# Optimization experiments

Measured on AMD Instinct MI355X. Metric: run time of the kernel, lower is better.

Reference implementation:

```python
import jax, jax.numpy as jnp
import numpy as np

B, S, D = 2, 2048, 768
H = 12
HD = D // H


def setup_inputs() -> dict:
    key = jax.random.key(0)
    ks = jax.random.split(key, 9)
    s_in = 1.0 / np.sqrt(D)
    return {
        "x": jax.random.normal(ks[0], (B, S, D), dtype=jnp.float32),
        "wq": jax.random.normal(ks[1], (D, D), dtype=jnp.float32) * s_in,
        "bq": jax.random.normal(ks[2], (D,), dtype=jnp.float32) * 0.01,
        "wk": jax.random.normal(ks[3], (D, D), dtype=jnp.float32) * s_in,
        "bk": jax.random.normal(ks[4], (D,), dtype=jnp.float32) * 0.01,
        "wv": jax.random.normal(ks[5], (D, D), dtype=jnp.float32) * s_in,
        "bv": jax.random.normal(ks[6], (D,), dtype=jnp.float32) * 0.01,
        "wo": jax.random.normal(ks[7], (D, D), dtype=jnp.float32) * s_in,
        "bo": jax.random.normal(ks[8], (D,), dtype=jnp.float32) * 0.01,
    }


def reference(x, wq, bq, wk, bk, wv, bv, wo, bo):
    b, s, _ = x.shape
    # projections -> [b, h, s, hd]
    def proj(w, bias):
        return (x @ w + bias).reshape(b, s, H, HD).transpose(0, 2, 1, 3)
    q = proj(wq, bq)
    k = proj(wk, bk)
    v = proj(wv, bv)
    scores = jnp.einsum("bhqd,bhkd->bhqk", q, k)
    causal = jnp.triu(jnp.ones((s, s), dtype=bool), k=1)
    scores = jnp.where(causal, -jnp.inf, scores)
    attn = jax.nn.softmax(scores / np.sqrt(HD), axis=-1)
    # dropout p=0.0 -> identity
    ctx = jnp.einsum("bhqk,bhkd->bhqd", attn, v)
    ctx = ctx.transpose(0, 2, 1, 3).reshape(b, s, D)
    return ctx @ wo + bo
```

## Files before the change

### kernel.cpp

```cpp
#include <hip/hip_runtime.h>
#include <math.h>

#define BB  2
#define SS  2048
#define DD  768
#define HH  12
#define HDD 64
#define BSR (BB * SS)
#define NCH 40
#define NKT 12

typedef __attribute__((ext_vector_type(8))) short bf16x8;
typedef __attribute__((ext_vector_type(4))) float f32x4;
typedef __attribute__((ext_vector_type(4))) int  i32x4;

__device__ inline f32x4 mfma16(bf16x8 a, bf16x8 b, f32x4 c) {
    return __builtin_amdgcn_mfma_f32_16x16x32_bf16(a, b, c, 0, 0, 0);
}

__device__ inline unsigned short f2b(float f) {
    unsigned int u = __float_as_uint(f);
    u += 0x7FFFu + ((u >> 16) & 1u);
    return (unsigned short)(u >> 16);
}
__device__ inline float b2f(unsigned short u) {
    return __uint_as_float((unsigned int)u << 16);
}

__device__ inline unsigned int cvt_pk_bf16(float lo, float hi) {
    unsigned int r;
    asm("v_cvt_pk_bf16_f32 %0, %1, %2" : "=v"(r) : "v"(lo), "v"(hi));
    return r;
}

__device__ inline void async_copy16(void* lds, const void* g) {
    __builtin_amdgcn_global_load_lds(
        (const __attribute__((address_space(1))) unsigned int*)g,
        (__attribute__((address_space(3))) unsigned int*)lds, 16, 0, 0);
}

__global__ __launch_bounds__(256) void conv_wT_kernel(
    const float* __restrict__ w0, const float* __restrict__ w1,
    const float* __restrict__ w2, const float* __restrict__ w3,
    unsigned short* __restrict__ o0, unsigned short* __restrict__ o1,
    unsigned short* __restrict__ o2, unsigned short* __restrict__ o3)
{
    const float* w = (blockIdx.z == 0) ? w0 : (blockIdx.z == 1) ? w1
                   : (blockIdx.z == 2) ? w2 : w3;
    unsigned short* o = (blockIdx.z == 0) ? o0 : (blockIdx.z == 1) ? o1
                      : (blockIdx.z == 2) ? o2 : o3;
    const int n0 = blockIdx.x * 64;
    const int k0 = blockIdx.y * 64;
    const int tid = threadIdx.x;

    __shared__ unsigned short tile[64][72];

#pragma unroll
    for (int p = 0; p < 4; ++p) {
        int c  = p * 256 + tid;
        int kr = c >> 4;
        int nc = (c & 15) * 4;
        float4 v = *(const float4*)&w[(size_t)(k0 + kr) * DD + n0 + nc];
        tile[nc + 0][kr] = f2b(v.x);
        tile[nc + 1][kr] = f2b(v.y);
        tile[nc + 2][kr] = f2b(v.z);
        tile[nc + 3][kr] = f2b(v.w);
    }
    __syncthreads();
#pragma unroll
    for (int p = 0; p < 2; ++p) {
        int c  = p * 256 + tid;
        int nr = c >> 3;
        int kc = (c & 7) * 8;
        *(i32x4*)&o[(size_t)(n0 + nr) * DD + k0 + kc] = *(const i32x4*)&tile[nr][kc];
    }
}

__global__ __launch_bounds__(256) void qkv_gemm_kernel(
    const float* __restrict__ x,
    const unsigned short* __restrict__ wqT, const unsigned short* __restrict__ wkT,
    const unsigned short* __restrict__ wvT,
    const float* __restrict__ bq, const float* __restrict__ bk,
    const float* __restrict__ bv,
    unsigned short* __restrict__ Qg, unsigned short* __restrict__ Kg,
    unsigned short* __restrict__ Vg)
{
    const int which = blockIdx.z;
    const unsigned short* Bt = (which == 0) ? wqT : (which == 1) ? wkT : wvT;
    const float* bias        = (which == 0) ? bq  : (which == 1) ? bk  : bv;
    unsigned short* out      = (which == 0) ? Qg  : (which == 1) ? Kg  : Vg;
    const float qs           = (which == 0) ? 0.18033688011112042f : 1.0f;

    const int m0 = blockIdx.x * 64;
    const int n0 = blockIdx.y * 128;
    const int tid  = threadIdx.x;
    const int w    = tid >> 6;
    const int lane = tid & 63;
    const int quad = lane >> 4;
    const int l16  = lane & 15;
    const int mh   = w & 1;
    const int nh   = w >> 1;
    const int swz  = l16 & 7;

    __shared__ unsigned short smem[24576];
    unsigned short (*As0)[64] = (unsigned short(*)[64])smem;
    unsigned short (*Bs0)[64] = (unsigned short(*)[64])(smem + 4096);
    unsigned short (*As1)[64] = (unsigned short(*)[64])(smem + 12288);
    unsigned short (*Bs1)[64] = (unsigned short(*)[64])(smem + 16384);
    unsigned short (*T)[136]  = (unsigned short(*)[136])smem;

    const int rA0 = tid >> 3,          jA0 = tid & 7,          chA0 = jA0 ^ (rA0 & 7);
    const int rA1 = (256 + tid) >> 3,  jA1 = tid & 7,          chA1 = jA1 ^ (rA1 & 7);
    const float* xr0 = &x[(size_t)(m0 + rA0) * DD + chA0 * 8];
    const float* xr1 = &x[(size_t)(m0 + rA1) * DD + chA1 * 8];
    int ldsA0 = rA0 * 64 + jA0 * 8;
    int ldsA1 = rA1 * 64 + jA1 * 8;

    const unsigned short* gB[4];
    int ldsB[4];
#pragma unroll
    for (int p = 0; p < 4; ++p) {
        int c  = p * 256 + tid;
        int r  = c >> 3;
        int j  = c & 7;
        int ch = j ^ (r & 7);
        gB[p]   = &Bt[(size_t)(n0 + r) * DD + ch * 8];
        ldsB[p] = r * 64 + j * 8;
    }

    f32x4 zero = {0.f, 0.f, 0.f, 0.f};
    f32x4 acc[2][4];
#pragma unroll
    for (int i = 0; i < 2; ++i)
#pragma unroll
        for (int j = 0; j < 4; ++j) acc[i][j] = zero;

    {
        float4 pf0 = *(const float4*)(xr0);
        float4 pf1 = *(const float4*)(xr0 + 4);
        float4 pf2 = *(const float4*)(xr1);
        float4 pf3 = *(const float4*)(xr1 + 4);
#pragma unroll
        for (int p = 0; p < 4; ++p)
            async_copy16((unsigned short*)Bs0 + ldsB[p], gB[p]);
        i32x4 tv;
        tv[0] = (int)cvt_pk_bf16(pf0.x, pf0.y);
        tv[1] = (int)cvt_pk_bf16(pf0.z, pf0.w);
        tv[2] = (int)cvt_pk_bf16(pf1.x, pf1.y);
        tv[3] = (int)cvt_pk_bf16(pf1.z, pf1.w);
        *(i32x4*)((unsigned short*)As0 + ldsA0) = tv;
        tv[0] = (int)cvt_pk_bf16(pf2.x, pf2.y);
        tv[1] = (int)cvt_pk_bf16(pf2.z, pf2.w);
        tv[2] = (int)cvt_pk_bf16(pf3.x, pf3.y);
        tv[3] = (int)cvt_pk_bf16(pf3.z, pf3.w);
        *(i32x4*)((unsigned short*)As0 + ldsA1) = tv;
    }
    __syncthreads();

#pragma unroll
    for (int t = 0; t < NKT; ++t) {
        const int kn = (t + 1) * 64;
        unsigned short (*As)[64] = (t & 1) ? As1 : As0;
        unsigned short (*Bs)[64] = (t & 1) ? Bs1 : Bs0;
        unsigned short (*An)[64] = (t & 1) ? As0 : As1;
        unsigned short (*Bn)[64] = (t & 1) ? Bs0 : Bs1;
        const bool more = (t + 1 < NKT);

        float4 pf0, pf1, pf2, pf3;
        if (more) {
            pf0 = *(const float4*)(xr0 + kn);
            pf1 = *(const float4*)(xr0 + kn + 4);
            pf2 = *(const float4*)(xr1 + kn);
            pf3 = *(const float4*)(xr1 + kn + 4);
#pragma unroll
            for (int p = 0; p < 4; ++p)
                async_copy16((unsigned short*)Bn + ldsB[p], gB[p] + kn);
        }

        bf16x8 af0[2], af1[2], bf0[4], bf1[4];
#pragma unroll
        for (int mt = 0; mt < 2; ++mt) {
            int r = mh * 32 + mt * 16 + l16;
            af0[mt] = *(const bf16x8*)&As[r][((quad    ) ^ swz) * 8];
            af1[mt] = *(const bf16x8*)&As[r][((quad + 4) ^ swz) * 8];
        }
#pragma unroll
        for (int nt = 0; nt < 4; ++nt) {
            int r = nh * 64 + nt * 16 + l16;
            bf0[nt] = *(const bf16x8*)&Bs[r][((quad    ) ^ swz) * 8];
            bf1[nt] = *(const bf16x8*)&Bs[r][((quad + 4) ^ swz) * 8];
        }
#pragma unroll
        for (int mt = 0; mt < 2; ++mt)
#pragma unroll
            for (int nt = 0; nt < 4; ++nt) {
                acc[mt][nt] = mfma16(af0[mt], bf0[nt], acc[mt][nt]);
                acc[mt][nt] = mfma16(af1[mt], bf1[nt], acc[mt][nt]);
            }

        if (more) {
            i32x4 tv;
            tv[0] = (int)cvt_pk_bf16(pf0.x, pf0.y);
            tv[1] = (int)cvt_pk_bf16(pf0.z, pf0.w);
            tv[2] = (int)cvt_pk_bf16(pf1.x, pf1.y);
            tv[3] = (int)cvt_pk_bf16(pf1.z, pf1.w);
            *(i32x4*)((unsigned short*)An + ldsA0) = tv;
            tv[0] = (int)cvt_pk_bf16(pf2.x, pf2.y);
            tv[1] = (int)cvt_pk_bf16(pf2.z, pf2.w);
            tv[2] = (int)cvt_pk_bf16(pf3.x, pf3.y);
            tv[3] = (int)cvt_pk_bf16(pf3.z, pf3.w);
            *(i32x4*)((unsigned short*)An + ldsA1) = tv;
        }
        __syncthreads();
    }

    if (which < 2) {
#pragma unroll
        for (int nt = 0; nt < 4; ++nt) {
            const int col = nh * 64 + nt * 16 + l16;
            const float bvv = bias[n0 + col];
#pragma unroll
            for (int mt = 0; mt < 2; ++mt)
#pragma unroll
                for (int r = 0; r < 4; ++r)
                    T[mh * 32 + mt * 16 + quad * 4 + r][col] =
                        f2b((acc[mt][nt][r] + bvv) * qs);
        }
        __syncthreads();
#pragma unroll
        for (int p2 = 0; p2 < 4; ++p2) {
            int c    = p2 * 256 + tid;
            int row  = c >> 4;
            int ck   = c & 15;
            int head = ck >> 3;
            int wi   = ck & 7;
            int sg   = m0 + row;
            int bi   = sg >> 11, si = sg & 2047;
            int hcol = (n0 >> 6) + head;
            *(i32x4*)&out[(((size_t)(bi * HH + hcol)) * SS + si) * HDD + wi * 8] =
                *(const i32x4*)&T[row][head * 64 + wi * 8];
        }
    } else {
        for (int pass = 0; pass < 2; ++pass) {
            if (pass) __syncthreads();
            if (nh == pass) {
#pragma unroll
                for (int nt = 0; nt < 4; ++nt) {
                    const float bvv = bias[n0 + pass * 64 + nt * 16 + l16];
#pragma unroll
                    for (int mt = 0; mt < 2; ++mt) {
                        uint2 pk;
                        pk.x = cvt_pk_bf16(acc[mt][nt][0] + bvv, acc[mt][nt][1] + bvv);
                        pk.y = cvt_pk_bf16(acc[mt][nt][2] + bvv, acc[mt][nt][3] + bvv);
                        *(uint2*)&T[nt * 16 + l16][mh * 32 + mt * 16 + quad * 4] = pk;
                    }
                }
            }
            __syncthreads();
            const int bi   = m0 >> 11;
            const int s0   = m0 & 2047;
            const int hcol = (n0 >> 6) + pass;
#pragma unroll
            for (int p2 = 0; p2 < 2; ++p2) {
                int c    = p2 * 256 + tid;
                int drow = c >> 3;
                int wi   = c & 7;
                *(i32x4*)&out[(((size_t)(bi * HH + hcol)) * HDD + drow) * SS + s0 + wi * 8] =
                    *(const i32x4*)&T[drow][wi * 8];
            }
        }
    }
}

__global__ __launch_bounds__(256) void out_gemm_kernel(
    const unsigned short* __restrict__ cb, const unsigned short* __restrict__ woT,
    const float* __restrict__ bo, float* __restrict__ out)
{
    const int m0 = blockIdx.x * 64;
    const int n0 = blockIdx.y * 128;
    const int tid  = threadIdx.x;
    const int w    = tid >> 6;
    const int lane = tid & 63;
    const int quad = lane >> 4;
    const int l16  = lane & 15;
    const int mh   = w & 1;
    const int nh   = w >> 1;
    const int swz  = l16 & 7;

    __shared__ unsigned short smem[24576];
    unsigned short (*As0)[64] = (unsigned short(*)[64])smem;
    unsigned short (*Bs0)[64] = (unsigned short(*)[64])(smem + 4096);
    unsigned short (*As1)[64] = (unsigned short(*)[64])(smem + 12288);
    unsigned short (*Bs1)[64] = (unsigned short(*)[64])(smem + 16384);

    const unsigned short* gA[2];
    int ldsA[2];
#pragma unroll
    for (int p = 0; p < 2; ++p) {
        int c  = p * 256 + tid;
        int r  = c >> 3;
        int j  = c & 7;
        int ch = j ^ (r & 7);
        gA[p]   = &cb[(size_t)(m0 + r) * DD + ch * 8];
        ldsA[p] = r * 64 + j * 8;
    }
    const unsigned short* gB[4];
    int ldsB[4];
#pragma unroll
    for (int p = 0; p < 4; ++p) {
        int c  = p * 256 + tid;
        int r  = c >> 3;
        int j  = c & 7;
        int ch = j ^ (r & 7);
        gB[p]   = &woT[(size_t)(n0 + r) * DD + ch * 8];
        ldsB[p] = r * 64 + j * 8;
    }

    f32x4 zero = {0.f, 0.f, 0.f, 0.f};
    f32x4 acc[2][4];
#pragma unroll
    for (int i = 0; i < 2; ++i)
#pragma unroll
        for (int j = 0; j < 4; ++j) acc[i][j] = zero;

#pragma unroll
    for (int p = 0; p < 2; ++p) async_copy16((unsigned short*)As0 + ldsA[p], gA[p]);
#pragma unroll
    for (int p = 0; p < 4; ++p) async_copy16((unsigned short*)Bs0 + ldsB[p], gB[p]);
    __syncthreads();

#pragma unroll
    for (int t = 0; t < NKT; ++t) {
        const int kn = (t + 1) * 64;
        unsigned short (*As)[64] = (t & 1) ? As1 : As0;
        unsigned short (*Bs)[64] = (t & 1) ? Bs1 : Bs0;
        unsigned short (*An)[64] = (t & 1) ? As0 : As1;
        unsigned short (*Bn)[64] = (t & 1) ? Bs0 : Bs1;
        if (t + 1 < NKT) {
#pragma unroll
            for (int p = 0; p < 2; ++p)
                async_copy16((unsigned short*)An + ldsA[p], gA[p] + kn);
#pragma unroll
            for (int p = 0; p < 4; ++p)
                async_copy16((unsigned short*)Bn + ldsB[p], gB[p] + kn);
        }
        bf16x8 af0[2], af1[2], bf0[4], bf1[4];
#pragma unroll
        for (int mt = 0; mt < 2; ++mt) {
            int r = mh * 32 + mt * 16 + l16;
            af0[mt] = *(const bf16x8*)&As[r][((quad    ) ^ swz) * 8];
            af1[mt] = *(const bf16x8*)&As[r][((quad + 4) ^ swz) * 8];
        }
#pragma unroll
        for (int nt = 0; nt < 4; ++nt) {
            int r = nh * 64 + nt * 16 + l16;
            bf0[nt] = *(const bf16x8*)&Bs[r][((quad    ) ^ swz) * 8];
            bf1[nt] = *(const bf16x8*)&Bs[r][((quad + 4) ^ swz) * 8];
        }
#pragma unroll
        for (int mt = 0; mt < 2; ++mt)
#pragma unroll
            for (int nt = 0; nt < 4; ++nt) {
                acc[mt][nt] = mfma16(af0[mt], bf0[nt], acc[mt][nt]);
                acc[mt][nt] = mfma16(af1[mt], bf1[nt], acc[mt][nt]);
            }
        __syncthreads();
    }

#pragma unroll
    for (int nt = 0; nt < 4; ++nt) {
        const int n = n0 + nh * 64 + nt * 16 + l16;
        const float bvv = bo[n];
#pragma unroll
        for (int mt = 0; mt < 2; ++mt) {
            const int mbase = m0 + mh * 32 + mt * 16 + quad * 4;
#pragma unroll
            for (int r = 0; r < 4; ++r)
                out[(size_t)(mbase + r) * DD + n] = acc[mt][nt][r] + bvv;
        }
    }
}

__global__ __launch_bounds__(256, 4) void attn_mfma_kernel(
    const unsigned short* __restrict__ Qg, const unsigned short* __restrict__ Kg,
    const unsigned short* __restrict__ Vg, unsigned short* __restrict__ Opart,
    float* __restrict__ Lb)
{
    const int c = (NCH - 1) - blockIdx.x;
    int qt, ck, nch;
    if (c < 4)       { qt = c;                            ck = 0;     nch = 1; }
    else if (c < 12) { int t = c - 4;  qt = 4  + (t >> 1); ck = t & 1; nch = 2; }
    else if (c < 24) { int t = c - 12; qt = 8  + t / 3;    ck = t % 3; nch = 3; }
    else             { int t = c - 24; qt = 12 + (t >> 2); ck = t & 3; nch = 4; }
    const int NT   = 2 * qt + 2;
    const int base = NT / nch, rem = NT % nch;
    const int lo   = ck * base + min(ck, rem);
    const int hi   = lo + base + (ck < rem ? 1 : 0);
    const int dlo  = 2 * qt;

    const int h  = blockIdx.y;
    const int b  = blockIdx.z;
    const int tid  = threadIdx.x;
    const int w    = tid >> 6;
    const int lane = tid & 63;
    const int quad = lane >> 4;
    const int l16  = lane & 15;
    const int q0   = qt * 128;

    const size_t bh = (size_t)(b * HH + h);
    const unsigned short* qp = Qg + bh * SS * HDD;
    const unsigned short* kp = Kg + bh * SS * HDD;
    const unsigned short* vp = Vg + bh * HDD * SS;

    unsigned short* op = Opart + ((size_t)bh * NCH + c) * 128 * HDD;
    float* lp = Lb + ((size_t)bh * NCH + c) * 128;

    __shared__ unsigned short Ks[64][64];
    __shared__ unsigned short Vt[64][64];
    __shared__ unsigned short PsT[4][2][16][72];
    unsigned short* slab = &PsT[w][0][0][0];

    bf16x8 qb0[2], qb1[2];
    int query[2];
#pragma unroll
    for (int qf = 0; qf < 2; ++qf) {
        query[qf] = q0 + w * 32 + qf * 16 + l16;
        qb0[qf] = *(const bf16x8*)&qp[(size_t)query[qf] * HDD + quad * 8];
        qb1[qf] = *(const bf16x8*)&qp[(size_t)query[qf] * HDD + 32 + quad * 8];
    }

    const int pr  = tid >> 3;
    const int po8 = tid & 7;
    const int fs  = l16 & 7;

    i32x4 kpre[2], vpre[2];
#pragma unroll
    for (int p = 0; p < 2; ++p) {
        int r  = pr + p * 32;
        int gc = (po8 ^ (r & 7)) * 8;
        kpre[p] = *(const i32x4*)&kp[(size_t)(lo * 64 + r) * HDD + gc];
        vpre[p] = *(const i32x4*)&vp[(size_t)r * SS + lo * 64 + gc];
    }

    f32x4 zero = {0.f, 0.f, 0.f, 0.f};
    f32x4 o_acc[2][4];
    float l_i[2] = {0.f, 0.f};
#pragma unroll
    for (int qf = 0; qf < 2; ++qf)
#pragma unroll
        for (int i = 0; i < 4; ++i) o_acc[qf][i] = zero;

    for (int kt = lo; kt < hi; ++kt) {
        const int k0 = kt * 64;
        __syncthreads();
#pragma unroll
        for (int p = 0; p < 2; ++p) {
            int r = pr + p * 32;
            *(i32x4*)&Ks[r][po8 * 8] = kpre[p];
            *(i32x4*)&Vt[r][po8 * 8] = vpre[p];
        }
        __syncthreads();

        if (kt + 1 < hi) {
            const int kn = (kt + 1) * 64;
#pragma unroll
            for (int p = 0; p < 2; ++p) {
                int r  = pr + p * 32;
                int gc = (po8 ^ (r & 7)) * 8;
                kpre[p] = *(const i32x4*)&kp[(size_t)(kn + r) * HDD + gc];
                vpre[p] = *(const i32x4*)&vp[(size_t)r * SS + kn + gc];
            }
        }

        const bool diag = (kt >= dlo);
#pragma unroll
        for (int t = 0; t < 4; ++t) {
            const int row = t * 16 + l16;
            bf16x8 klo = *(const bf16x8*)&Ks[row][((quad    ) ^ fs) * 8];
            bf16x8 khi = *(const bf16x8*)&Ks[row][((quad + 4) ^ fs) * 8];
#pragma unroll
            for (int qf = 0; qf < 2; ++qf) {
                f32x4 s = mfma16(klo, qb0[qf], zero);
                s = mfma16(khi, qb1[qf], s);
                float pv[4];
#pragma unroll
                for (int r = 0; r < 4; ++r) {
                    const int key = k0 + t * 16 + quad * 4 + r;
                    float p = exp2f(s[r]);
                    if (diag && key > query[qf]) p = 0.f;
                    pv[r] = p;
                    l_i[qf] += p;
                }
                uint2 pk;
                pk.x = cvt_pk_bf16(pv[0], pv[1]);
                pk.y = cvt_pk_bf16(pv[2], pv[3]);
                *(uint2*)&slab[(qf * 16 + l16) * 72 + t * 16 + quad * 4] = pk;
            }
        }

        bf16x8 pb0[2], pb1[2];
#pragma unroll
        for (int qf = 0; qf < 2; ++qf) {
            pb0[qf] = *(const bf16x8*)&slab[(qf * 16 + l16) * 72 + quad * 8];
            pb1[qf] = *(const bf16x8*)&slab[(qf * 16 + l16) * 72 + 32 + quad * 8];
        }
#pragma unroll
        for (int t2 = 0; t2 < 4; ++t2) {
            const int row = t2 * 16 + l16;
            bf16x8 vlo = *(const bf16x8*)&Vt[row][((quad    ) ^ fs) * 8];
            bf16x8 vhi = *(const bf16x8*)&Vt[row][((quad + 4) ^ fs) * 8];
#pragma unroll
            for (int qf = 0; qf < 2; ++qf) {
                o_acc[qf][t2] = mfma16(vlo, pb0[qf], o_acc[qf][t2]);
                o_acc[qf][t2] = mfma16(vhi, pb1[qf], o_acc[qf][t2]);
            }
        }
    }

#pragma unroll
    for (int qf = 0; qf < 2; ++qf) {
        float l = l_i[qf];
        l += __shfl_xor(l, 16);
        l += __shfl_xor(l, 32);
        if (quad == 0) lp[w * 32 + qf * 16 + l16] = l;
#pragma unroll
        for (int t2 = 0; t2 < 4; ++t2) {
            uint2 pk;
            pk.x = cvt_pk_bf16(o_acc[qf][t2][0], o_acc[qf][t2][1]);
            pk.y = cvt_pk_bf16(o_acc[qf][t2][2], o_acc[qf][t2][3]);
            *(uint2*)&slab[(qf * 16 + l16) * 72 + t2 * 16 + quad * 4] = pk;
        }
    }
#pragma unroll
    for (int p2 = 0; p2 < 4; ++p2) {
        int cc  = p2 * 64 + lane;
        int row = cc >> 3, dc = cc & 7;
        *(i32x4*)&op[(size_t)(w * 32 + row) * HDD + dc * 8] =
            *(const i32x4*)&slab[row * 72 + dc * 8];
    }
}

__global__ __launch_bounds__(256) void merge_kernel(
    const unsigned short* __restrict__ Opart, const float* __restrict__ Lb,
    unsigned short* __restrict__ cb)
{
    const int bx   = blockIdx.x;
    const int qt2  = bx >> 1;
    const int half = bx & 1;
    const int bhn  = blockIdx.y;
    const int b    = bhn / HH, h = bhn % HH;
    const int tid  = threadIdx.x;
    const int row  = tid >> 2;
    const int d0   = (tid & 3) * 16;
    const int rowc = half * 64 + row;
    const int q    = qt2 * 128 + rowc;

    const int nch = (qt2 < 4) ? 1 : (qt2 < 8) ? 2 : (qt2 < 12) ? 3 : 4;
    const int cb0 = (qt2 < 4) ? qt2
                  : (qt2 < 8)  ? (4  + (qt2 - 4)  * 2)
                  : (qt2 < 12) ? (12 + (qt2 - 8)  * 3)
                  :              (24 + (qt2 - 12) * 4);

    float suml = 0.f;
    float accv[16];
#pragma unroll
    for (int i = 0; i < 16; ++i) accv[i] = 0.f;

    for (int ci = 0; ci < nch; ++ci) {
        const size_t base = (size_t)bhn * NCH + cb0 + ci;
        suml += Lb[base * 128 + rowc];
        const unsigned short* o = Opart + (base * 128 + rowc) * HDD + d0;
        i32x4 va = *(const i32x4*)&o[0];
        i32x4 vb = *(const i32x4*)&o[8];
#pragma unroll
        for (int wd = 0; wd < 4; ++wd) {
            unsigned int ua = (unsigned int)va[wd];
            accv[wd * 2 + 0] += __uint_as_float(ua << 16);
            accv[wd * 2 + 1] += __uint_as_float(ua & 0xffff0000u);
            unsigned int ub = (unsigned int)vb[wd];
            accv[8 + wd * 2 + 0] += __uint_as_float(ub << 16);
            accv[8 + wd * 2 + 1] += __uint_as_float(ub & 0xffff0000u);
        }
    }
    const float inv = 1.0f / suml;
    unsigned int res[8];
#pragma unroll
    for (int i = 0; i < 8; ++i)
        res[i] = cvt_pk_bf16(accv[2 * i] * inv, accv[2 * i + 1] * inv);
    unsigned short* dst = &cb[((size_t)(b * SS + q)) * DD + h * HDD + d0];
    *(i32x4*)&dst[0] = *(const i32x4*)&res[0];
    *(i32x4*)&dst[8] = *(const i32x4*)&res[4];
}

extern "C" void kernel_launch(void* const* d_in, const int* in_sizes, int n_in,
                              void* d_out, int out_size, void* d_ws, size_t ws_size,
                              hipStream_t stream)
{
    const float* x  = (const float*)d_in[0];
    const float* wq = (const float*)d_in[1];
    const float* bq = (const float*)d_in[2];
    const float* wk = (const float*)d_in[3];
    const float* bk = (const float*)d_in[4];
    const float* wv = (const float*)d_in[5];
    const float* bv = (const float*)d_in[6];
    const float* wo = (const float*)d_in[7];
    const float* bo = (const float*)d_in[8];
    float* out = (float*)d_out;

    char* p = (char*)d_ws;
    const size_t XB  = (size_t)BSR * DD * 2;
    const size_t WB  = (size_t)DD * DD * 2;
    const size_t OPB = (size_t)BB * HH * NCH * 128 * HDD * 2;
    const size_t LBB = (size_t)BB * HH * NCH * 128 * 4;
    unsigned short* wqT = (unsigned short*)p;            p += WB;
    unsigned short* wkT = (unsigned short*)p;            p += WB;
    unsigned short* wvT = (unsigned short*)p;            p += WB;
    unsigned short* woT = (unsigned short*)p;            p += WB;
    unsigned short* Qg  = (unsigned short*)p;            p += XB;
    unsigned short* Kg  = (unsigned short*)p;            p += XB;
    unsigned short* Vg  = (unsigned short*)p;            p += XB;
    unsigned short* cb  = (unsigned short*)p;            p += XB;
    unsigned short* Opart = (unsigned short*)p;          p += OPB;
    float* Lb = (float*)p;                               p += LBB;

    conv_wT_kernel<<<dim3(DD / 64, DD / 64, 4), 256, 0, stream>>>(
        wq, wk, wv, wo, wqT, wkT, wvT, woT);
    qkv_gemm_kernel<<<dim3(BSR / 64, DD / 128, 3), 256, 0, stream>>>(
        x, wqT, wkT, wvT, bq, bk, bv, Qg, Kg, Vg);
    attn_mfma_kernel<<<dim3(NCH, HH, BB), 256, 0, stream>>>(
        Qg, Kg, Vg, Opart, Lb);
    merge_kernel<<<dim3(32, BB * HH), 256, 0, stream>>>(Opart, Lb, cb);
    out_gemm_kernel<<<dim3(BSR / 64, DD / 128), 256, 0, stream>>>(cb, woT, bo, out);
}
```

Before: 162.9 us.

## Pre-convert x to bf16 and remap GEMM/attention blocks for XCD locality

Adds a separate kernel that converts x to bf16 once, so the QKV GEMM can load A tiles with async global-to-LDS copies instead of converting float registers inside the loop. It also flattens the grids of the QKV GEMM, attention and output GEMM kernels. Block IDs are remapped so that consecutive blocks on the same XCD share M tiles or batch-head slices, aiming for better L2 reuse. The cost is one extra launch and an extra round trip of x through memory.

```diff
diff --git a/kernel.cpp b/kernel.cpp
--- a/kernel.cpp
+++ b/kernel.cpp
@@ -37,6 +37,20 @@
     __builtin_amdgcn_global_load_lds(
         (const __attribute__((address_space(1))) unsigned int*)g,
         (__attribute__((address_space(3))) unsigned int*)lds, 16, 0, 0);
+}
+
+__global__ __launch_bounds__(256) void conv_x_kernel(
+    const float* __restrict__ x, unsigned short* __restrict__ xb)
+{
+    const size_t i = ((size_t)blockIdx.x * 256 + threadIdx.x) * 8;
+    float4 f0 = *(const float4*)&x[i];
+    float4 f1 = *(const float4*)&x[i + 4];
+    i32x4 tv;
+    tv[0] = (int)cvt_pk_bf16(f0.x, f0.y);
+    tv[1] = (int)cvt_pk_bf16(f0.z, f0.w);
+    tv[2] = (int)cvt_pk_bf16(f1.x, f1.y);
+    tv[3] = (int)cvt_pk_bf16(f1.z, f1.w);
+    *(i32x4*)&xb[i] = tv;
 }
 
 __global__ __launch_bounds__(256) void conv_wT_kernel(
@@ -77,7 +91,7 @@
 }
 
 __global__ __launch_bounds__(256) void qkv_gemm_kernel(
-    const float* __restrict__ x,
+    const unsigned short* __restrict__ xb,
     const unsigned short* __restrict__ wqT, const unsigned short* __restrict__ wkT,
     const unsigned short* __restrict__ wvT,
     const float* __restrict__ bq, const float* __restrict__ bk,
@@ -85,14 +99,21 @@
     unsigned short* __restrict__ Qg, unsigned short* __restrict__ Kg,
     unsigned short* __restrict__ Vg)
 {
-    const int which = blockIdx.z;
+    const int p0   = blockIdx.x;
+    const int xcd  = p0 & 7;
+    const int slot = p0 >> 3;
+    const int m_t  = (slot / 18) * 8 + xcd;
+    const int nw   = slot % 18;
+    const int n_t  = nw / 3;
+    const int which = nw % 3;
+
     const unsigned short* Bt = (which == 0) ? wqT : (which == 1) ? wkT : wvT;
     const float* bias        = (which == 0) ? bq  : (which == 1) ? bk  : bv;
     unsigned short* out      = (which == 0) ? Qg  : (which == 1) ? Kg  : Vg;
     const float qs           = (which == 0) ? 0.18033688011112042f : 1.0f;
 
-    const int m0 = blockIdx.x * 64;
-    const int n0 = blockIdx.y * 128;
+    const int m0 = m_t * 64;
+    const int n0 = n_t * 128;
     const int tid  = threadIdx.x;
     const int w    = tid >> 6;
     const int lane = tid & 63;
@@ -109,13 +130,17 @@
     unsigned short (*Bs1)[64] = (unsigned short(*)[64])(smem + 16384);
     unsigned short (*T)[136]  = (unsigned short(*)[136])smem;
 
-    const int rA0 = tid >> 3,          jA0 = tid & 7,          chA0 = jA0 ^ (rA0 & 7);
-    const int rA1 = (256 + tid) >> 3,  jA1 = tid & 7,          chA1 = jA1 ^ (rA1 & 7);
-    const float* xr0 = &x[(size_t)(m0 + rA0) * DD + chA0 * 8];
-    const float* xr1 = &x[(size_t)(m0 + rA1) * DD + chA1 * 8];
-    int ldsA0 = rA0 * 64 + jA0 * 8;
-    int ldsA1 = rA1 * 64 + jA1 * 8;
-
+    const unsigned short* gA[2];
+    int ldsA[2];
+#pragma unroll
+    for (int p = 0; p < 2; ++p) {
+        int c  = p * 256 + tid;
+        int r  = c >> 3;
+        int j  = c & 7;
+        int ch = j ^ (r & 7);
+        gA[p]   = &xb[(size_t)(m0 + r) * DD + ch * 8];
+        ldsA[p] = r * 64 + j * 8;
+    }
     const unsigned short* gB[4];
     int ldsB[4];
 #pragma unroll
@@ -135,26 +160,10 @@
 #pragma unroll
         for (int j = 0; j < 4; ++j) acc[i][j] = zero;
 
-    {
-        float4 pf0 = *(const float4*)(xr0);
-        float4 pf1 = *(const float4*)(xr0 + 4);
-        float4 pf2 = *(const float4*)(xr1);
-        float4 pf3 = *(const float4*)(xr1 + 4);
-#pragma unroll
-        for (int p = 0; p < 4; ++p)
-            async_copy16((unsigned short*)Bs0 + ldsB[p], gB[p]);
-        i32x4 tv;
-        tv[0] = (int)cvt_pk_bf16(pf0.x, pf0.y);
-        tv[1] = (int)cvt_pk_bf16(pf0.z, pf0.w);
-        tv[2] = (int)cvt_pk_bf16(pf1.x, pf1.y);
-        tv[3] = (int)cvt_pk_bf16(pf1.z, pf1.w);
-        *(i32x4*)((unsigned short*)As0 + ldsA0) = tv;
-        tv[0] = (int)cvt_pk_bf16(pf2.x, pf2.y);
-        tv[1] = (int)cvt_pk_bf16(pf2.z, pf2.w);
-        tv[2] = (int)cvt_pk_bf16(pf3.x, pf3.y);
-        tv[3] = (int)cvt_pk_bf16(pf3.z, pf3.w);
-        *(i32x4*)((unsigned short*)As0 + ldsA1) = tv;
-    }
+#pragma unroll
+    for (int p = 0; p < 2; ++p) async_copy16((unsigned short*)As0 + ldsA[p], gA[p]);
+#pragma unroll
+    for (int p = 0; p < 4; ++p) async_copy16((unsigned short*)Bs0 + ldsB[p], gB[p]);
     __syncthreads();
 
 #pragma unroll
@@ -164,19 +173,14 @@
         unsigned short (*Bs)[64] = (t & 1) ? Bs1 : Bs0;
         unsigned short (*An)[64] = (t & 1) ? As0 : As1;
         unsigned short (*Bn)[64] = (t & 1) ? Bs0 : Bs1;
-        const bool more = (t + 1 < NKT);
-
-        float4 pf0, pf1, pf2, pf3;
-        if (more) {
-            pf0 = *(const float4*)(xr0 + kn);
-            pf1 = *(const float4*)(xr0 + kn + 4);
-            pf2 = *(const float4*)(xr1 + kn);
-            pf3 = *(const float4*)(xr1 + kn + 4);
+        if (t + 1 < NKT) {
+#pragma unroll
+            for (int p = 0; p < 2; ++p)
+                async_copy16((unsigned short*)An + ldsA[p], gA[p] + kn);
 #pragma unroll
             for (int p = 0; p < 4; ++p)
                 async_copy16((unsigned short*)Bn + ldsB[p], gB[p] + kn);
         }
-
         bf16x8 af0[2], af1[2], bf0[4], bf1[4];
 #pragma unroll
         for (int mt = 0; mt < 2; ++mt) {
@@ -197,20 +201,6 @@
                 acc[mt][nt] = mfma16(af0[mt], bf0[nt], acc[mt][nt]);
                 acc[mt][nt] = mfma16(af1[mt], bf1[nt], acc[mt][nt]);
             }
-
-        if (more) {
-            i32x4 tv;
-            tv[0] = (int)cvt_pk_bf16(pf0.x, pf0.y);
-            tv[1] = (int)cvt_pk_bf16(pf0.z, pf0.w);
-            tv[2] = (int)cvt_pk_bf16(pf1.x, pf1.y);
-            tv[3] = (int)cvt_pk_bf16(pf1.z, pf1.w);
-            *(i32x4*)((unsigned short*)An + ldsA0) = tv;
-            tv[0] = (int)cvt_pk_bf16(pf2.x, pf2.y);
-            tv[1] = (int)cvt_pk_bf16(pf2.z, pf2.w);
-            tv[2] = (int)cvt_pk_bf16(pf3.x, pf3.y);
-            tv[3] = (int)cvt_pk_bf16(pf3.z, pf3.w);
-            *(i32x4*)((unsigned short*)An + ldsA1) = tv;
-        }
         __syncthreads();
     }
 
@@ -276,8 +266,11 @@
     const unsigned short* __restrict__ cb, const unsigned short* __restrict__ woT,
     const float* __restrict__ bo, float* __restrict__ out)
 {
-    const int m0 = blockIdx.x * 64;
-    const int n0 = blockIdx.y * 128;
+    const int p0   = blockIdx.x;
+    const int xcd  = p0 & 7;
+    const int slot = p0 >> 3;
+    const int m0 = ((slot / 6) * 8 + xcd) * 64;
+    const int n0 = (slot % 6) * 128;
     const int tid  = threadIdx.x;
     const int w    = tid >> 6;
     const int lane = tid & 63;
@@ -386,7 +379,14 @@
     const unsigned short* __restrict__ Vg, unsigned short* __restrict__ Opart,
     float* __restrict__ Lb)
 {
-    const int c = (NCH - 1) - blockIdx.x;
+    const int p0   = blockIdx.x;
+    const int xcd  = p0 & 7;
+    const int slot = p0 >> 3;
+    const int bh_i = (slot / 40) * 8 + xcd;
+    const int b    = bh_i / HH;
+    const int h    = bh_i % HH;
+    const int c    = (NCH - 1) - (slot % 40);
+
     int qt, ck, nch;
     if (c < 4)       { qt = c;                            ck = 0;     nch = 1; }
     else if (c < 12) { int t = c - 4;  qt = 4  + (t >> 1); ck = t & 1; nch = 2; }
@@ -398,8 +398,6 @@
     const int hi   = lo + base + (ck < rem ? 1 : 0);
     const int dlo  = 2 * qt;
 
-    const int h  = blockIdx.y;
-    const int b  = blockIdx.z;
     const int tid  = threadIdx.x;
     const int w    = tid >> 6;
     const int lane = tid & 63;
@@ -407,7 +405,7 @@
     const int l16  = lane & 15;
     const int q0   = qt * 128;
 
-    const size_t bh = (size_t)(b * HH + h);
+    const size_t bh = (size_t)bh_i;
     const unsigned short* qp = Qg + bh * SS * HDD;
     const unsigned short* kp = Kg + bh * SS * HDD;
     const unsigned short* vp = Vg + bh * HDD * SS;
@@ -616,6 +614,7 @@
     unsigned short* wkT = (unsigned short*)p;            p += WB;
     unsigned short* wvT = (unsigned short*)p;            p += WB;
     unsigned short* woT = (unsigned short*)p;            p += WB;
+    unsigned short* xb  = (unsigned short*)p;            p += XB;
     unsigned short* Qg  = (unsigned short*)p;            p += XB;
     unsigned short* Kg  = (unsigned short*)p;            p += XB;
     unsigned short* Vg  = (unsigned short*)p;            p += XB;
@@ -623,12 +622,13 @@
     unsigned short* Opart = (unsigned short*)p;          p += OPB;
     float* Lb = (float*)p;                               p += LBB;
 
+    conv_x_kernel<<<dim3(BSR * DD / (256 * 8)), 256, 0, stream>>>(x, xb);
     conv_wT_kernel<<<dim3(DD / 64, DD / 64, 4), 256, 0, stream>>>(
         wq, wk, wv, wo, wqT, wkT, wvT, woT);
-    qkv_gemm_kernel<<<dim3(BSR / 64, DD / 128, 3), 256, 0, stream>>>(
-        x, wqT, wkT, wvT, bq, bk, bv, Qg, Kg, Vg);
-    attn_mfma_kernel<<<dim3(NCH, HH, BB), 256, 0, stream>>>(
+    qkv_gemm_kernel<<<dim3(1152), 256, 0, stream>>>(
+        xb, wqT, wkT, wvT, bq, bk, bv, Qg, Kg, Vg);
+    attn_mfma_kernel<<<dim3(960), 256, 0, stream>>>(
         Qg, Kg, Vg, Opart, Lb);
     merge_kernel<<<dim3(32, BB * HH), 256, 0, stream>>>(Opart, Lb, cb);
-    out_gemm_kernel<<<dim3(BSR / 64, DD / 128), 256, 0, stream>>>(cb, woT, bo, out);
-}
+    out_gemm_kernel<<<dim3(384), 256, 0, stream>>>(cb, woT, bo, out);
+}
```

Result: faster. 153.2 us (-6.0%).
